# Kernel tuning notes

Hardware: AMD Instinct MI355X
Metric: run time of the kernel (lower is better)

The kernel has to match this reference:

```python
import jax, jax.numpy as jnp
import numpy as np
import math

B, C, H, W = 8, 256, 64, 64
G = 32           # norm_groups
IMG_C = 3        # image_channels * wavelet_components
EPS = 1e-5


def group_norm(x, gamma, beta):
    # x: [B, C, H, W]; normalize over (C//G, H, W) within each of G groups
    b, c, h, w = x.shape
    xg = x.reshape(b, G, c // G, h, w)
    mean = xg.mean(axis=(2, 3, 4), keepdims=True)
    var = xg.var(axis=(2, 3, 4), keepdims=True)
    xg = (xg - mean) * jax.lax.rsqrt(var + EPS)
    x = xg.reshape(b, c, h, w)
    return x * gamma[None, :, None, None] + beta[None, :, None, None]


def conv1x1(x, weight):
    # weight: [out_c, in_c]; 1x1 conv == channel matmul
    return jnp.einsum('oc,bchw->bohw', weight, x)


def setup_inputs() -> dict:
    key = jax.random.key(0)
    ks = jax.random.split(key, 8)
    s_q = 1.0 / math.sqrt(IMG_C)
    s_kv = 1.0 / math.sqrt(C)
    return {
        'input': jax.random.normal(ks[0], (B, C, H, W), jnp.float32),
        'quary': jax.random.normal(ks[1], (B, IMG_C, H, W), jnp.float32),
        'gn_weight': jnp.ones((C,), jnp.float32),
        'gn_bias': jnp.zeros((C,), jnp.float32),
        'w_q': jax.random.uniform(ks[2], (C, IMG_C), jnp.float32, -s_q, s_q),
        'w_kv': jax.random.uniform(ks[3], (2 * C, C), jnp.float32, -s_kv, s_kv),
        'w_out': jax.random.uniform(ks[4], (C, C), jnp.float32, -s_kv, s_kv),
        'b_out': jax.random.uniform(ks[5], (C,), jnp.float32, -s_kv, s_kv),
    }


def reference(input, quary, gn_weight, gn_bias, w_q, w_kv, w_out, b_out):
    b, c, h, w = input.shape
    norm = group_norm(input, gn_weight, gn_bias)
    kv = conv1x1(norm, w_kv)                      # [B, 2C, H, W]
    key_t, value = kv[:, :c], kv[:, c:]           # each [B, C, H, W]
    q = conv1x1(quary, w_q)                       # [B, C, H, W]
    # attention over all spatial positions, single head, head_dim = C
    attn = jnp.einsum('bchw,bcyx->bhwyx', q, key_t) / math.sqrt(c)
    attn = jax.nn.softmax(attn.reshape(b, h, w, h * w), axis=-1)
    attn = attn.reshape(b, h, w, h, w)
    out = jnp.einsum('bhwyx,bcyx->bchw', attn, value)  # [B, C, H, W]
    out = conv1x1(out, w_out) + b_out[None, :, None, None]
    return out + input
```

## Files before the change

kernel.cpp:

```cpp
#include <hip/hip_runtime.h>

typedef unsigned short u16;
typedef unsigned int   u32;
typedef float  f32x4  __attribute__((ext_vector_type(4)));
typedef float  fltx4  __attribute__((ext_vector_type(4)));
typedef float  f32x2  __attribute__((ext_vector_type(2)));
typedef short  bf16x8 __attribute__((ext_vector_type(8)));
typedef u32    u32x4  __attribute__((ext_vector_type(4)));
typedef u32    u32x2  __attribute__((ext_vector_type(2)));

#define CDIM 256
#define NPIX 4096
#define QSCALE 0.09016843736f

__device__ __forceinline__ u16 f2bf(float f) {
  u32 u = __builtin_bit_cast(u32, f);
  u += 0x7fffu + ((u >> 16) & 1u);
  return (u16)(u >> 16);
}
__device__ __forceinline__ float bf2f(u16 h) {
  return __builtin_bit_cast(float, (u32)h << 16);
}

#if __has_builtin(__builtin_amdgcn_exp2f)
#define FEXP2 __builtin_amdgcn_exp2f
#else
#define FEXP2 exp2f
#endif

#define LO2(v) __builtin_shufflevector(v, v, 0, 1)
#define HI2(v) __builtin_shufflevector(v, v, 2, 3)

union U8 { bf16x8 v; u16 u[8]; u32 w[4]; };

__device__ __forceinline__ void llds16(u16* lds_base, const u16* gsrc) {
  __builtin_amdgcn_global_load_lds(
      (const __attribute__((address_space(1))) unsigned int*)gsrc,
      (__attribute__((address_space(3))) unsigned int*)lds_base, 16, 0, 0);
}

__global__ __launch_bounds__(256) void prep(const float* __restrict__ wkv,
                                            const float* __restrict__ wout,
                                            const float* __restrict__ wq,
                                            u16* __restrict__ w16,
                                            float* __restrict__ wq3p) {
  const int blk = blockIdx.x, tid = threadIdx.x;
  if (blk < 4) {
    const float* s = (blk < 2 ? wkv + 65536 : wout) + (blk & 1) * 32768;
    u16* d = w16 + (blk >> 1) * 65536 + (blk & 1) * 32768;
    for (int i = tid * 4; i < 32768; i += 1024) {
      fltx4 v = *(const fltx4*)(s + i);
      u32x2 o;
      o[0] = (u32)f2bf(v[0]) | ((u32)f2bf(v[1]) << 16);
      o[1] = (u32)f2bf(v[2]) | ((u32)f2bf(v[3]) << 16);
      *(u32x2*)(d + i) = o;
    }
  } else {
    const int p = blk - 4, c = tid;
    float a0 = 0.f, a1 = 0.f, a2 = 0.f;
    for (int o = p * 64; o < p * 64 + 64; ++o) {
      float kv = wkv[o * 256 + c];
      a0 += wq[o * 3 + 0] * kv;
      a1 += wq[o * 3 + 1] * kv;
      a2 += wq[o * 3 + 2] * kv;
    }
    float* dst = wq3p + (p * 256 + c) * 4;
    dst[0] = a0 * QSCALE; dst[1] = a1 * QSCALE; dst[2] = a2 * QSCALE; dst[3] = 0.f;
  }
}

__global__ __launch_bounds__(1024) void gn_stats(const float* __restrict__ x,
                                                 float* __restrict__ stats) {
  int bg = blockIdx.x;
  const float* base = x + (long)bg * 32768;
  float s = 0.f, s2 = 0.f;
  for (int i = threadIdx.x; i < 8192; i += 1024) {
    fltx4 v = ((const fltx4*)base)[i];
    s  += v[0] + v[1] + v[2] + v[3];
    s2 += v[0]*v[0] + v[1]*v[1] + v[2]*v[2] + v[3]*v[3];
  }
  for (int off = 1; off < 64; off <<= 1) {
    s  += __shfl_xor(s, off);
    s2 += __shfl_xor(s2, off);
  }
  __shared__ float red[32];
  int w = threadIdx.x >> 6;
  if ((threadIdx.x & 63) == 0) { red[w] = s; red[16 + w] = s2; }
  __syncthreads();
  if (threadIdx.x < 16) {
    s  = red[threadIdx.x];
    s2 = red[16 + threadIdx.x];
    for (int off = 1; off < 16; off <<= 1) {
      s  += __shfl_xor(s, off);
      s2 += __shfl_xor(s2, off);
    }
    if (threadIdx.x == 0) {
      float mean = s * (1.f / 32768.f);
      float var  = s2 * (1.f / 32768.f) - mean * mean;
      stats[bg * 2]     = mean;
      stats[bg * 2 + 1] = rsqrtf(var + 1e-5f);
    }
  }
}

__global__ __launch_bounds__(256) void gn_apply(const float* __restrict__ x,
                                                const float* __restrict__ stats,
                                                const float* __restrict__ gamma,
                                                const float* __restrict__ beta,
                                                const float* __restrict__ wq3p,
                                                u16* __restrict__ normT,
                                                float* __restrict__ K3x,
                                                float* __restrict__ K3y,
                                                float* __restrict__ K3z) {
  __shared__ u16 tile[256 * 66];
  __shared__ float wl4[256 * 4];
  __shared__ float part[4][64][4];
  const int tid = threadIdx.x;
  const int b = blockIdx.y, nb = blockIdx.x * 64;
  const int nIn = tid & 63, c4 = tid >> 6;
  {
    const f32x4* wp = (const f32x4*)wq3p;
    *(f32x4*)&wl4[tid * 4] = wp[tid] + wp[256 + tid] + wp[512 + tid] + wp[768 + tid];
  }
  const float* xb = x + (long)b * (CDIM * NPIX);
  #pragma unroll 4
  for (int p = 0; p < 64; ++p) {
    int c = c4 * 64 + p;
    int g = c >> 3;
    float mean = stats[(b * 32 + g) * 2];
    float rstd = stats[(b * 32 + g) * 2 + 1];
    float v = xb[(long)c * NPIX + nb + nIn];
    tile[c * 66 + nIn] = f2bf((v - mean) * rstd * gamma[c] + beta[c]);
  }
  __syncthreads();
  u16* nT = normT + ((long)b * NPIX + nb) * CDIM;
  #pragma unroll 8
  for (int nl = 0; nl < 64; ++nl)
    nT[(long)nl * CDIM + tid] = tile[tid * 66 + nl];
  {
    float a0 = 0.f, a1 = 0.f, a2 = 0.f;
    #pragma unroll 8
    for (int cc = 0; cc < 64; ++cc) {
      int c = c4 * 64 + cc;
      float v = bf2f(tile[c * 66 + nIn]);
      const f32x4 wv = *(const f32x4*)&wl4[c * 4];
      a0 += v * wv[0]; a1 += v * wv[1]; a2 += v * wv[2];
    }
    part[c4][nIn][0] = a0; part[c4][nIn][1] = a1; part[c4][nIn][2] = a2;
  }
  __syncthreads();
  if (c4 == 0) {
    float s0 = part[0][nIn][0] + part[1][nIn][0] + part[2][nIn][0] + part[3][nIn][0];
    float s1 = part[0][nIn][1] + part[1][nIn][1] + part[2][nIn][1] + part[3][nIn][1];
    float s2 = part[0][nIn][2] + part[1][nIn][2] + part[2][nIn][2] + part[3][nIn][2];
    long idx = (long)b * NPIX + nb + nIn;
    K3x[idx] = s0; K3y[idx] = s1; K3z[idx] = s2;
  }
}

template <bool FINAL, bool MERGE>
__global__ __launch_bounds__(256, 2) void gemm_nt(
    const void* __restrict__ Ap, const void* __restrict__ Bp,
    const void* __restrict__ Bp2, const float* __restrict__ ls,
    void* __restrict__ Dp,
    const float* __restrict__ bias, const float* __restrict__ resid,
    int M, int N, long aBS, long bBS, long dBS, long rBS) {
  __shared__ u16 Als[128 * 72];
  __shared__ u16 Bls[128 * 72];
  __shared__ float invB[128];
  const int tid = threadIdx.x;
  const int lane = tid & 63;
  const int m = lane & 15, quad = lane >> 4;
  const int wid = tid >> 6;
  const int wm = wid & 1, wn = wid >> 1;
  const int m0 = blockIdx.x * 128, n0 = blockIdx.y * 128;
  const int bz = blockIdx.z;

  if constexpr (MERGE) {
    if (tid < 128) {
      long n = (long)bz * 4096 + n0 + tid;
      invB[tid] = 1.f / (ls[n] + ls[32768 + n]);
    }
    __syncthreads();
  }

  f32x4 acc[4][4] = {};

  for (int ks = 0; ks < 4; ++ks) {
    const int kb = ks * 64;
    if (ks) __syncthreads();
    {
      const u16* src = (const u16*)Ap + aBS * bz;
      #pragma unroll
      for (int it = 0; it < 4; ++it) {
        int idx = it * 2048 + tid * 8;
        int r = idx >> 6, c = idx & 63;
        *(u32x4*)&Als[r * 72 + c] = *(const u32x4*)(src + (long)(m0 + r) * CDIM + kb + c);
      }
    }
    if constexpr (MERGE) {
      const u16* s0 = (const u16*)Bp  + bBS * bz;
      const u16* s1 = (const u16*)Bp2 + bBS * bz;
      #pragma unroll
      for (int it = 0; it < 4; ++it) {
        int idx = it * 2048 + tid * 8;
        int r = idx >> 6, c = idx & 63;
        long off = (long)(n0 + r) * CDIM + kb + c;
        u32x4 A  = *(const u32x4*)(s0 + off);
        u32x4 Bq = *(const u32x4*)(s1 + off);
        float inv = invB[r];
        u32x4 o;
        #pragma unroll
        for (int i = 0; i < 4; ++i) {
          float lo = (bf2f((u16)(A[i] & 0xffff)) + bf2f((u16)(Bq[i] & 0xffff))) * inv;
          float hi = (bf2f((u16)(A[i] >> 16))    + bf2f((u16)(Bq[i] >> 16)))    * inv;
          o[i] = (u32)f2bf(lo) | ((u32)f2bf(hi) << 16);
        }
        *(u32x4*)&Bls[r * 72 + c] = o;
      }
    } else {
      const u16* src = (const u16*)Bp + bBS * bz;
      #pragma unroll
      for (int it = 0; it < 4; ++it) {
        int idx = it * 2048 + tid * 8;
        int r = idx >> 6, c = idx & 63;
        *(u32x4*)&Bls[r * 72 + c] = *(const u32x4*)(src + (long)(n0 + r) * CDIM + kb + c);
      }
    }
    __syncthreads();
    #pragma unroll
    for (int s = 0; s < 2; ++s) {
      bf16x8 av[4], bv[4];
      #pragma unroll
      for (int i = 0; i < 4; ++i)
        av[i] = *(const bf16x8*)&Als[(wm * 64 + i * 16 + m) * 72 + s * 32 + quad * 8];
      #pragma unroll
      for (int i = 0; i < 4; ++i)
        bv[i] = *(const bf16x8*)&Bls[(wn * 64 + i * 16 + m) * 72 + s * 32 + quad * 8];
      #pragma unroll
      for (int mi = 0; mi < 4; ++mi)
        #pragma unroll
        for (int ni = 0; ni < 4; ++ni)
          acc[mi][ni] = __builtin_amdgcn_mfma_f32_16x16x32_bf16(av[mi], bv[ni], acc[mi][ni], 0, 0, 0);
    }
  }

  const int row0 = m0 + wm * 64;
  const int col0 = n0 + wn * 64 + m;
  if constexpr (FINAL) {
    float* out = (float*)Dp + dBS * bz;
    const float* res = resid + rBS * bz;
    #pragma unroll
    for (int mi = 0; mi < 4; ++mi)
      #pragma unroll
      for (int r = 0; r < 4; ++r) {
        int row = row0 + mi * 16 + quad * 4 + r;
        float bs = bias[row];
        #pragma unroll
        for (int ni = 0; ni < 4; ++ni) {
          long off = (long)row * N + col0 + ni * 16;
          out[off] = acc[mi][ni][r] + bs + res[off];
        }
      }
  } else {
    u16* out = (u16*)Dp + dBS * bz;
    #pragma unroll
    for (int mi = 0; mi < 4; ++mi)
      #pragma unroll
      for (int r = 0; r < 4; ++r) {
        int row = row0 + mi * 16 + quad * 4 + r;
        #pragma unroll
        for (int ni = 0; ni < 4; ++ni)
          out[(long)row * N + col0 + ni * 16] = f2bf(acc[mi][ni][r]);
      }
  }
}

#define MFMA16(a, bfr, c) __builtin_amdgcn_mfma_f32_16x16x32_bf16(a, bfr, c, 0, 0, 0)

#define PH_LOAD(ks, h)                                                      \
  {                                                                         \
    const int jo_ = JB + (ks) * 32 + quad * 8 + (h) * 4;                    \
    kxa = *(const fltx4*)(Kx + jo_);                                        \
    kya = *(const fltx4*)(Ky + jo_);                                        \
    kza = *(const fltx4*)(Kz + jo_);                                        \
  }

#define PH_EXP(PB, ks, h)                                                   \
  {                                                                         \
    f32x2 xc0_ = LO2(kxa), xc1_ = HI2(kxa);                                 \
    f32x2 yc0_ = LO2(kya), yc1_ = HI2(kya);                                 \
    f32x2 zc0_ = LO2(kza), zc1_ = HI2(kza);                                 \
    f32x2 s0_ = xc0_ * y2[0] + yc0_ * y2[1] + zc0_ * y2[2];                 \
    f32x2 s1_ = xc1_ * y2[0] + yc1_ * y2[1] + zc1_ * y2[2];                 \
    float p0_ = FEXP2(s0_[0]);                                              \
    float p1_ = FEXP2(s0_[1]);                                              \
    float p2_ = FEXP2(s1_[0]);                                              \
    float p3_ = FEXP2(s1_[1]);                                              \
    u32 r0_ = __builtin_bit_cast(u32, p0_) + 0x8000u;                       \
    u32 r1_ = __builtin_bit_cast(u32, p1_) + 0x8000u;                       \
    u32 r2_ = __builtin_bit_cast(u32, p2_) + 0x8000u;                       \
    u32 r3_ = __builtin_bit_cast(u32, p3_) + 0x8000u;                       \
    PB[ks].w[(h) * 2]     = (r0_ >> 16) | (r1_ & 0xffff0000u);              \
    PB[ks].w[(h) * 2 + 1] = (r2_ >> 16) | (r3_ & 0xffff0000u);              \
    f32x2 pa_; pa_[0] = p0_; pa_[1] = p1_;                                  \
    f32x2 pb_; pb_[0] = p2_; pb_[1] = p3_;                                  \
    lsv += pa_ + pb_;                                                       \
  }

#define PV_G(PB, CT0)                                                       \
  _Pragma("unroll")                                                         \
  for (int ct_ = (CT0); ct_ < (CT0) + 4; ++ct_) {                           \
    int c_ = ct_ * 16 + m;                                                  \
    bf16x8 a0_ = *(const bf16x8*)&Vb[c_ * 64 + (((quad)     ^ (c_ & 7)) << 3)]; \
    bf16x8 a1_ = *(const bf16x8*)&Vb[c_ * 64 + (((4 + quad) ^ (c_ & 7)) << 3)]; \
    acc[ct_] = MFMA16(a0_, PB[0].v, acc[ct_]);                              \
    acc[ct_] = MFMA16(a1_, PB[1].v, acc[ct_]);                              \
  }

__global__ __launch_bounds__(512, 4) void attn_kernel(
    const float* __restrict__ quary,
    const float* __restrict__ K3x, const float* __restrict__ K3y,
    const float* __restrict__ K3z,
    const u16* __restrict__ V, u16* __restrict__ Op0, u16* __restrict__ Op1,
    float* __restrict__ lsum) {
  __shared__ u16 VLS[2][256 * 64];
  const int lane = threadIdx.x & 63, w = threadIdx.x >> 6;
  const int m = lane & 15, quad = lane >> 4;
  const int b = blockIdx.z, half = blockIdx.y;
  const int qb = blockIdx.x * 128 + w * 16;

  f32x2 y2[3];
  {
    int n = qb + m;
    float q0 = quary[b * 12288 + n];
    float q1 = quary[b * 12288 + 4096 + n];
    float q2 = quary[b * 12288 + 8192 + n];
    y2[0][0] = q0; y2[0][1] = q0;
    y2[1][0] = q1; y2[1][1] = q1;
    y2[2][0] = q2; y2[2][1] = q2;
  }

  const float* Kx = K3x + (long)b * NPIX + half * 2048;
  const float* Ky = K3y + (long)b * NPIX + half * 2048;
  const float* Kz = K3z + (long)b * NPIX + half * 2048;
  const u16* VG = V + (long)b * CDIM * NPIX + half * 2048;

  int srcV[4];
  #pragma unroll
  for (int i = 0; i < 4; ++i) {
    int c = (w * 4 + i) * 8 + (lane >> 3);
    srcV[i] = c * NPIX + (((lane & 7) ^ (c & 7)) << 3);
  }

  f32x2 lsv = {};
  f32x4 acc[16] = {};
  U8 pbA[2], pbB[2];
  fltx4 kxa, kya, kza;

  #pragma unroll
  for (int i = 0; i < 4; ++i)
    llds16(VLS[0] + (w * 4 + i) * 512, VG + srcV[i]);

  {
    const int JB = 0;
    PH_LOAD(0, 0); PH_EXP(pbA, 0, 0);
    PH_LOAD(0, 1); PH_EXP(pbA, 0, 1);
    PH_LOAD(1, 0); PH_EXP(pbA, 1, 0);
    PH_LOAD(1, 1); PH_EXP(pbA, 1, 1);
  }

  for (int kt = 0; kt < 31; ++kt) {
    __syncthreads();
    #pragma unroll
    for (int i = 0; i < 4; ++i)
      llds16(VLS[(kt + 1) & 1] + (w * 4 + i) * 512, VG + srcV[i] + (kt + 1) * 64);
    const u16* Vb = VLS[kt & 1];
    const int JB = (kt + 1) * 64;

    PH_LOAD(0, 0);
    PV_G(pbA, 0);
    PH_EXP(pbB, 0, 0);
    PH_LOAD(0, 1);
    PV_G(pbA, 4);
    PH_EXP(pbB, 0, 1);
    PH_LOAD(1, 0);
    PV_G(pbA, 8);
    PH_EXP(pbB, 1, 0);
    PH_LOAD(1, 1);
    PV_G(pbA, 12);
    PH_EXP(pbB, 1, 1);

    pbA[0] = pbB[0]; pbA[1] = pbB[1];
  }
  {
    __syncthreads();
    const u16* Vb = VLS[1];
    PV_G(pbA, 0);
    PV_G(pbA, 4);
    PV_G(pbA, 8);
    PV_G(pbA, 12);
  }

  u16* OpB = (half ? Op1 : Op0);
  {
    int n = qb + m;
    u16* row = OpB + ((long)b * NPIX + n) * CDIM + quad * 4;
    #pragma unroll
    for (int ct = 0; ct < 16; ++ct) {
      u32x2 o;
      o[0] = (u32)f2bf(acc[ct][0]) | ((u32)f2bf(acc[ct][1]) << 16);
      o[1] = (u32)f2bf(acc[ct][2]) | ((u32)f2bf(acc[ct][3]) << 16);
      *(u32x2*)(row + ct * 16) = o;
    }
    float ls = lsv[0] + lsv[1];
    ls += __shfl_xor(ls, 16);
    ls += __shfl_xor(ls, 32);
    if (lane < 16)
      lsum[(long)half * 32768 + (long)b * NPIX + n] = ls;
  }
}

extern "C" void kernel_launch(void* const* d_in, const int* in_sizes, int n_in,
                              void* d_out, int out_size, void* d_ws, size_t ws_size,
                              hipStream_t stream) {
  (void)in_sizes; (void)n_in; (void)out_size; (void)ws_size;
  const float* input = (const float*)d_in[0];
  const float* quary = (const float*)d_in[1];
  const float* gnw   = (const float*)d_in[2];
  const float* gnb   = (const float*)d_in[3];
  const float* wq    = (const float*)d_in[4];
  const float* wkv   = (const float*)d_in[5];
  const float* wout  = (const float*)d_in[6];
  const float* bout  = (const float*)d_in[7];
  float* out = (float*)d_out;

  char* ws = (char*)d_ws;
  float* stats = (float*)ws;
  float* wq3p  = (float*)(ws + 4096);
  float* lsum  = (float*)(ws + 20480);
  float* K3x   = (float*)(ws + 282624);
  float* K3y   = (float*)(ws + 413696);
  float* K3z   = (float*)(ws + 544768);
  u16* w16   = (u16*)(ws + 675840);
  u16* normT = (u16*)(ws + 937984);
  u16* Vv    = (u16*)(ws + 937984 + 1L * 16777216);
  u16* Op0   = normT;
  u16* Op1   = (u16*)(ws + 937984 + 2L * 16777216);

  const long S = (long)NPIX * CDIM;

  prep<<<8, 256, 0, stream>>>(wkv, wout, wq, w16, wq3p);
  gn_stats<<<256, 1024, 0, stream>>>(input, stats);
  gn_apply<<<dim3(64, 8), 256, 0, stream>>>(input, stats, gnw, gnb, wq3p,
                                            normT, K3x, K3y, K3z);
  gemm_nt<false, false><<<dim3(2, 32, 8), 256, 0, stream>>>(
      w16, normT, nullptr, nullptr, Vv, nullptr, nullptr, 256, 4096, 0, S, S, 0);
  attn_kernel<<<dim3(32, 2, 8), 512, 0, stream>>>(quary, K3x, K3y, K3z, Vv, Op0, Op1, lsum);
  gemm_nt<true, true><<<dim3(2, 32, 8), 256, 0, stream>>>(
      w16 + 65536, Op0, Op1, lsum, out, bout, input, 256, 4096, 0, S, S, S);
}
```

Measured before the change: 261.2 us.

## Split attention KV range four ways with smaller V tiles and two query tiles per wave

The attention kernel now processes 32 query rows per wave (two 16-row MFMA tiles sharing each V fragment) with 256-thread blocks and 32-wide KV tiles, halving LDS per block. When the workspace is large enough, the KV dimension is split four ways instead of two, with a 4-way merge of partial outputs and row sums in the output GEMM. This aims to raise occupancy and V-fragment reuse, at the cost of more partial-output traffic (two extra 16 MB bf16 buffers written and read) and more accumulator registers.

```diff
diff --git a/kernel.cpp b/kernel.cpp
--- a/kernel.cpp
+++ b/kernel.cpp
@@ -158,10 +158,12 @@
   }
 }
 
-template <bool FINAL, bool MERGE>
+template <bool FINAL, int WAYS>
 __global__ __launch_bounds__(256, 2) void gemm_nt(
-    const void* __restrict__ Ap, const void* __restrict__ Bp,
-    const void* __restrict__ Bp2, const float* __restrict__ ls,
+    const void* __restrict__ Ap,
+    const void* __restrict__ B0, const void* __restrict__ B1,
+    const void* __restrict__ B2, const void* __restrict__ B3,
+    const float* __restrict__ ls,
     void* __restrict__ Dp,
     const float* __restrict__ bias, const float* __restrict__ resid,
     int M, int N, long aBS, long bBS, long dBS, long rBS) {
@@ -176,10 +178,12 @@
   const int m0 = blockIdx.x * 128, n0 = blockIdx.y * 128;
   const int bz = blockIdx.z;
 
-  if constexpr (MERGE) {
+  if constexpr (WAYS > 0) {
     if (tid < 128) {
       long n = (long)bz * 4096 + n0 + tid;
-      invB[tid] = 1.f / (ls[n] + ls[32768 + n]);
+      float s = ls[n] + ls[32768 + n];
+      if constexpr (WAYS == 4) s += ls[65536 + n] + ls[98304 + n];
+      invB[tid] = 1.f / s;
     }
     __syncthreads();
   }
@@ -198,28 +202,40 @@
         *(u32x4*)&Als[r * 72 + c] = *(const u32x4*)(src + (long)(m0 + r) * CDIM + kb + c);
       }
     }
-    if constexpr (MERGE) {
-      const u16* s0 = (const u16*)Bp  + bBS * bz;
-      const u16* s1 = (const u16*)Bp2 + bBS * bz;
+    if constexpr (WAYS > 0) {
+      const u16* s0 = (const u16*)B0 + bBS * bz;
+      const u16* s1 = (const u16*)B1 + bBS * bz;
+      const u16* s2 = (const u16*)B2 + bBS * bz;
+      const u16* s3 = (const u16*)B3 + bBS * bz;
       #pragma unroll
       for (int it = 0; it < 4; ++it) {
         int idx = it * 2048 + tid * 8;
         int r = idx >> 6, c = idx & 63;
         long off = (long)(n0 + r) * CDIM + kb + c;
-        u32x4 A  = *(const u32x4*)(s0 + off);
-        u32x4 Bq = *(const u32x4*)(s1 + off);
+        u32x4 A0 = *(const u32x4*)(s0 + off);
+        u32x4 A1 = *(const u32x4*)(s1 + off);
+        u32x4 A2 = {}, A3 = {};
+        if constexpr (WAYS == 4) {
+          A2 = *(const u32x4*)(s2 + off);
+          A3 = *(const u32x4*)(s3 + off);
+        }
         float inv = invB[r];
         u32x4 o;
         #pragma unroll
         for (int i = 0; i < 4; ++i) {
-          float lo = (bf2f((u16)(A[i] & 0xffff)) + bf2f((u16)(Bq[i] & 0xffff))) * inv;
-          float hi = (bf2f((u16)(A[i] >> 16))    + bf2f((u16)(Bq[i] >> 16)))    * inv;
+          float lo = bf2f((u16)(A0[i] & 0xffff)) + bf2f((u16)(A1[i] & 0xffff));
+          float hi = bf2f((u16)(A0[i] >> 16))    + bf2f((u16)(A1[i] >> 16));
+          if constexpr (WAYS == 4) {
+            lo += bf2f((u16)(A2[i] & 0xffff)) + bf2f((u16)(A3[i] & 0xffff));
+            hi += bf2f((u16)(A2[i] >> 16))    + bf2f((u16)(A3[i] >> 16));
+          }
+          lo *= inv; hi *= inv;
           o[i] = (u32)f2bf(lo) | ((u32)f2bf(hi) << 16);
         }
         *(u32x4*)&Bls[r * 72 + c] = o;
       }
     } else {
-      const u16* src = (const u16*)Bp + bBS * bz;
+      const u16* src = (const u16*)B0 + bBS * bz;
       #pragma unroll
       for (int it = 0; it < 4; ++it) {
         int idx = it * 2048 + tid * 8;
@@ -278,83 +294,91 @@
 
 #define MFMA16(a, bfr, c) __builtin_amdgcn_mfma_f32_16x16x32_bf16(a, bfr, c, 0, 0, 0)
 
-#define PH_LOAD(ks, h)                                                      \
+#define PH_LOAD(h)                                                          \
   {                                                                         \
-    const int jo_ = JB + (ks) * 32 + quad * 8 + (h) * 4;                    \
+    const int jo_ = JB + quad * 8 + (h) * 4;                                \
     kxa = *(const fltx4*)(Kx + jo_);                                        \
     kya = *(const fltx4*)(Ky + jo_);                                        \
     kza = *(const fltx4*)(Kz + jo_);                                        \
   }
 
-#define PH_EXP(PB, ks, h)                                                   \
+#define PH_EXP(PB, h)                                                       \
   {                                                                         \
     f32x2 xc0_ = LO2(kxa), xc1_ = HI2(kxa);                                 \
     f32x2 yc0_ = LO2(kya), yc1_ = HI2(kya);                                 \
     f32x2 zc0_ = LO2(kza), zc1_ = HI2(kza);                                 \
-    f32x2 s0_ = xc0_ * y2[0] + yc0_ * y2[1] + zc0_ * y2[2];                 \
-    f32x2 s1_ = xc1_ * y2[0] + yc1_ * y2[1] + zc1_ * y2[2];                 \
-    float p0_ = FEXP2(s0_[0]);                                              \
-    float p1_ = FEXP2(s0_[1]);                                              \
-    float p2_ = FEXP2(s1_[0]);                                              \
-    float p3_ = FEXP2(s1_[1]);                                              \
-    u32 r0_ = __builtin_bit_cast(u32, p0_) + 0x8000u;                       \
-    u32 r1_ = __builtin_bit_cast(u32, p1_) + 0x8000u;                       \
-    u32 r2_ = __builtin_bit_cast(u32, p2_) + 0x8000u;                       \
-    u32 r3_ = __builtin_bit_cast(u32, p3_) + 0x8000u;                       \
-    PB[ks].w[(h) * 2]     = (r0_ >> 16) | (r1_ & 0xffff0000u);              \
-    PB[ks].w[(h) * 2 + 1] = (r2_ >> 16) | (r3_ & 0xffff0000u);              \
-    f32x2 pa_; pa_[0] = p0_; pa_[1] = p1_;                                  \
-    f32x2 pb_; pb_[0] = p2_; pb_[1] = p3_;                                  \
-    lsv += pa_ + pb_;                                                       \
+    _Pragma("unroll")                                                       \
+    for (int qm_ = 0; qm_ < 2; ++qm_) {                                     \
+      f32x2 s0_ = xc0_ * y2[qm_][0] + yc0_ * y2[qm_][1] + zc0_ * y2[qm_][2];\
+      f32x2 s1_ = xc1_ * y2[qm_][0] + yc1_ * y2[qm_][1] + zc1_ * y2[qm_][2];\
+      float p0_ = FEXP2(s0_[0]);                                            \
+      float p1_ = FEXP2(s0_[1]);                                            \
+      float p2_ = FEXP2(s1_[0]);                                            \
+      float p3_ = FEXP2(s1_[1]);                                            \
+      u32 r0_ = __builtin_bit_cast(u32, p0_) + 0x8000u;                     \
+      u32 r1_ = __builtin_bit_cast(u32, p1_) + 0x8000u;                     \
+      u32 r2_ = __builtin_bit_cast(u32, p2_) + 0x8000u;                     \
+      u32 r3_ = __builtin_bit_cast(u32, p3_) + 0x8000u;                     \
+      PB[qm_].w[(h) * 2]     = (r0_ >> 16) | (r1_ & 0xffff0000u);           \
+      PB[qm_].w[(h) * 2 + 1] = (r2_ >> 16) | (r3_ & 0xffff0000u);           \
+      f32x2 pa_; pa_[0] = p0_; pa_[1] = p1_;                                \
+      f32x2 pc_; pc_[0] = p2_; pc_[1] = p3_;                                \
+      lsv[qm_] += pa_ + pc_;                                                \
+    }                                                                       \
   }
 
 #define PV_G(PB, CT0)                                                       \
   _Pragma("unroll")                                                         \
   for (int ct_ = (CT0); ct_ < (CT0) + 4; ++ct_) {                           \
     int c_ = ct_ * 16 + m;                                                  \
-    bf16x8 a0_ = *(const bf16x8*)&Vb[c_ * 64 + (((quad)     ^ (c_ & 7)) << 3)]; \
-    bf16x8 a1_ = *(const bf16x8*)&Vb[c_ * 64 + (((4 + quad) ^ (c_ & 7)) << 3)]; \
-    acc[ct_] = MFMA16(a0_, PB[0].v, acc[ct_]);                              \
-    acc[ct_] = MFMA16(a1_, PB[1].v, acc[ct_]);                              \
-  }
-
-__global__ __launch_bounds__(512, 4) void attn_kernel(
+    bf16x8 a_ = *(const bf16x8*)&Vb[c_ * 32 + ((quad ^ ((c_ >> 1) & 3)) << 3)]; \
+    acc[0][ct_] = MFMA16(a_, PB[0].v, acc[0][ct_]);                         \
+    acc[1][ct_] = MFMA16(a_, PB[1].v, acc[1][ct_]);                         \
+  }
+
+template <int NT>
+__global__ __launch_bounds__(256, 4) void attn_kernel(
     const float* __restrict__ quary,
     const float* __restrict__ K3x, const float* __restrict__ K3y,
     const float* __restrict__ K3z,
-    const u16* __restrict__ V, u16* __restrict__ Op0, u16* __restrict__ Op1,
+    const u16* __restrict__ V,
+    u16* __restrict__ Op0, u16* __restrict__ Op1,
+    u16* __restrict__ Op2, u16* __restrict__ Op3,
     float* __restrict__ lsum) {
-  __shared__ u16 VLS[2][256 * 64];
+  __shared__ u16 VLS[2][256 * 32];
   const int lane = threadIdx.x & 63, w = threadIdx.x >> 6;
   const int m = lane & 15, quad = lane >> 4;
-  const int b = blockIdx.z, half = blockIdx.y;
-  const int qb = blockIdx.x * 128 + w * 16;
-
-  f32x2 y2[3];
-  {
-    int n = qb + m;
+  const int b = blockIdx.z, way = blockIdx.y;
+  const int qb = blockIdx.x * 128 + w * 32;
+  const int kv0 = way * (NT * 32);
+
+  f32x2 y2[2][3];
+  #pragma unroll
+  for (int qm = 0; qm < 2; ++qm) {
+    int n = qb + qm * 16 + m;
     float q0 = quary[b * 12288 + n];
     float q1 = quary[b * 12288 + 4096 + n];
     float q2 = quary[b * 12288 + 8192 + n];
-    y2[0][0] = q0; y2[0][1] = q0;
-    y2[1][0] = q1; y2[1][1] = q1;
-    y2[2][0] = q2; y2[2][1] = q2;
-  }
-
-  const float* Kx = K3x + (long)b * NPIX + half * 2048;
-  const float* Ky = K3y + (long)b * NPIX + half * 2048;
-  const float* Kz = K3z + (long)b * NPIX + half * 2048;
-  const u16* VG = V + (long)b * CDIM * NPIX + half * 2048;
+    y2[qm][0][0] = q0; y2[qm][0][1] = q0;
+    y2[qm][1][0] = q1; y2[qm][1][1] = q1;
+    y2[qm][2][0] = q2; y2[qm][2][1] = q2;
+  }
+
+  const float* Kx = K3x + (long)b * NPIX + kv0;
+  const float* Ky = K3y + (long)b * NPIX + kv0;
+  const float* Kz = K3z + (long)b * NPIX + kv0;
+  const u16* VG = V + (long)b * CDIM * NPIX + kv0;
 
   int srcV[4];
   #pragma unroll
   for (int i = 0; i < 4; ++i) {
-    int c = (w * 4 + i) * 8 + (lane >> 3);
-    srcV[i] = c * NPIX + (((lane & 7) ^ (c & 7)) << 3);
-  }
-
-  f32x2 lsv = {};
-  f32x4 acc[16] = {};
+    int c = (w * 4 + i) * 16 + (lane >> 2);
+    int s = lane & 3;
+    srcV[i] = c * NPIX + ((s ^ ((c >> 1) & 3)) << 3);
+  }
+
+  f32x2 lsv[2] = {};
+  f32x4 acc[2][16] = {};
   U8 pbA[2], pbB[2];
   fltx4 kxa, kya, kza;
 
@@ -364,67 +388,62 @@
 
   {
     const int JB = 0;
-    PH_LOAD(0, 0); PH_EXP(pbA, 0, 0);
-    PH_LOAD(0, 1); PH_EXP(pbA, 0, 1);
-    PH_LOAD(1, 0); PH_EXP(pbA, 1, 0);
-    PH_LOAD(1, 1); PH_EXP(pbA, 1, 1);
-  }
-
-  for (int kt = 0; kt < 31; ++kt) {
+    PH_LOAD(0); PH_EXP(pbA, 0);
+    PH_LOAD(1); PH_EXP(pbA, 1);
+  }
+
+  for (int kt = 0; kt < NT - 1; ++kt) {
     __syncthreads();
     #pragma unroll
     for (int i = 0; i < 4; ++i)
-      llds16(VLS[(kt + 1) & 1] + (w * 4 + i) * 512, VG + srcV[i] + (kt + 1) * 64);
+      llds16(VLS[(kt + 1) & 1] + (w * 4 + i) * 512, VG + srcV[i] + (kt + 1) * 32);
     const u16* Vb = VLS[kt & 1];
-    const int JB = (kt + 1) * 64;
-
-    PH_LOAD(0, 0);
+    const int JB = (kt + 1) * 32;
+
+    PH_LOAD(0);
     PV_G(pbA, 0);
-    PH_EXP(pbB, 0, 0);
-    PH_LOAD(0, 1);
     PV_G(pbA, 4);
-    PH_EXP(pbB, 0, 1);
-    PH_LOAD(1, 0);
+    PH_EXP(pbB, 0);
+    PH_LOAD(1);
     PV_G(pbA, 8);
-    PH_EXP(pbB, 1, 0);
-    PH_LOAD(1, 1);
     PV_G(pbA, 12);
-    PH_EXP(pbB, 1, 1);
+    PH_EXP(pbB, 1);
 
     pbA[0] = pbB[0]; pbA[1] = pbB[1];
   }
   {
     __syncthreads();
-    const u16* Vb = VLS[1];
+    const u16* Vb = VLS[(NT - 1) & 1];
     PV_G(pbA, 0);
     PV_G(pbA, 4);
     PV_G(pbA, 8);
     PV_G(pbA, 12);
   }
 
-  u16* OpB = (half ? Op1 : Op0);
-  {
-    int n = qb + m;
+  u16* OpB = (way == 0) ? Op0 : (way == 1) ? Op1 : (way == 2) ? Op2 : Op3;
+  #pragma unroll
+  for (int qm = 0; qm < 2; ++qm) {
+    int n = qb + qm * 16 + m;
     u16* row = OpB + ((long)b * NPIX + n) * CDIM + quad * 4;
     #pragma unroll
     for (int ct = 0; ct < 16; ++ct) {
       u32x2 o;
-      o[0] = (u32)f2bf(acc[ct][0]) | ((u32)f2bf(acc[ct][1]) << 16);
-      o[1] = (u32)f2bf(acc[ct][2]) | ((u32)f2bf(acc[ct][3]) << 16);
+      o[0] = (u32)f2bf(acc[qm][ct][0]) | ((u32)f2bf(acc[qm][ct][1]) << 16);
+      o[1] = (u32)f2bf(acc[qm][ct][2]) | ((u32)f2bf(acc[qm][ct][3]) << 16);
       *(u32x2*)(row + ct * 16) = o;
     }
-    float ls = lsv[0] + lsv[1];
+    float ls = lsv[qm][0] + lsv[qm][1];
     ls += __shfl_xor(ls, 16);
     ls += __shfl_xor(ls, 32);
     if (lane < 16)
-      lsum[(long)half * 32768 + (long)b * NPIX + n] = ls;
+      lsum[(long)way * 32768 + (long)b * NPIX + n] = ls;
   }
 }
 
 extern "C" void kernel_launch(void* const* d_in, const int* in_sizes, int n_in,
                               void* d_out, int out_size, void* d_ws, size_t ws_size,
                               hipStream_t stream) {
-  (void)in_sizes; (void)n_in; (void)out_size; (void)ws_size;
+  (void)in_sizes; (void)n_in; (void)out_size;
   const float* input = (const float*)d_in[0];
   const float* quary = (const float*)d_in[1];
   const float* gnw   = (const float*)d_in[2];
@@ -439,14 +458,19 @@
   float* stats = (float*)ws;
   float* wq3p  = (float*)(ws + 4096);
   float* lsum  = (float*)(ws + 20480);
-  float* K3x   = (float*)(ws + 282624);
-  float* K3y   = (float*)(ws + 413696);
-  float* K3z   = (float*)(ws + 544768);
-  u16* w16   = (u16*)(ws + 675840);
-  u16* normT = (u16*)(ws + 937984);
-  u16* Vv    = (u16*)(ws + 937984 + 1L * 16777216);
+  float* K3x   = (float*)(ws + 544768);
+  float* K3y   = (float*)(ws + 675840);
+  float* K3z   = (float*)(ws + 806912);
+  u16* w16   = (u16*)(ws + 937984);
+  const long base = 1200128;
+  u16* normT = (u16*)(ws + base);
+  u16* Vv    = (u16*)(ws + base + 1L * 16777216);
   u16* Op0   = normT;
-  u16* Op1   = (u16*)(ws + 937984 + 2L * 16777216);
+  u16* Op1   = (u16*)(ws + base + 2L * 16777216);
+  u16* Op2   = (u16*)(ws + base + 3L * 16777216);
+  u16* Op3   = (u16*)(ws + base + 4L * 16777216);
+  const size_t need4 = (size_t)base + 5ul * 16777216ul;
+  const int ways = (ws_size >= need4) ? 4 : 2;
 
   const long S = (long)NPIX * CDIM;
 
@@ -454,9 +478,20 @@
   gn_stats<<<256, 1024, 0, stream>>>(input, stats);
   gn_apply<<<dim3(64, 8), 256, 0, stream>>>(input, stats, gnw, gnb, wq3p,
                                             normT, K3x, K3y, K3z);
-  gemm_nt<false, false><<<dim3(2, 32, 8), 256, 0, stream>>>(
-      w16, normT, nullptr, nullptr, Vv, nullptr, nullptr, 256, 4096, 0, S, S, 0);
-  attn_kernel<<<dim3(32, 2, 8), 512, 0, stream>>>(quary, K3x, K3y, K3z, Vv, Op0, Op1, lsum);
-  gemm_nt<true, true><<<dim3(2, 32, 8), 256, 0, stream>>>(
-      w16 + 65536, Op0, Op1, lsum, out, bout, input, 256, 4096, 0, S, S, S);
-}
+  gemm_nt<false, 0><<<dim3(2, 32, 8), 256, 0, stream>>>(
+      w16, normT, nullptr, nullptr, nullptr, nullptr, Vv, nullptr, nullptr,
+      256, 4096, 0, S, S, 0);
+  if (ways == 4) {
+    attn_kernel<32><<<dim3(32, 4, 8), 256, 0, stream>>>(
+        quary, K3x, K3y, K3z, Vv, Op0, Op1, Op2, Op3, lsum);
+    gemm_nt<true, 4><<<dim3(2, 32, 8), 256, 0, stream>>>(
+        w16 + 65536, Op0, Op1, Op2, Op3, lsum, out, bout, input,
+        256, 4096, 0, S, S, S);
+  } else {
+    attn_kernel<64><<<dim3(32, 2, 8), 256, 0, stream>>>(
+        quary, K3x, K3y, K3z, Vv, Op0, Op1, Op2, Op3, lsum);
+    gemm_nt<true, 2><<<dim3(2, 32, 8), 256, 0, stream>>>(
+        w16 + 65536, Op0, Op1, Op2, Op3, lsum, out, bout, input,
+        256, 4096, 0, S, S, S);
+  }
+}
```

Result: slower. 664.6 us (+154.5%).
